# Optimization experiments

Hardware: AMD Instinct MI355X
Metric: run time of the kernel (lower is better)

The kernel has to match this reference:

```python
import jax, jax.numpy as jnp
import numpy as np

NUM_SLICES = 16
FEAT = 512  # last-dim size of input


def setup_inputs() -> dict:
    key = jax.random.key(0)
    k1, k2 = jax.random.split(key)
    input_tensor = jax.random.normal(k1, (2048, 64, FEAT), dtype=jnp.float32)
    # 16 slice start offsets, each slice of length 64 stays within FEAT
    slices_index = jnp.sort(jax.random.randint(k2, (NUM_SLICES,), 0, 448)).astype(jnp.int32)
    return {"input_tensor": input_tensor, "slices_index": slices_index, "slice_len": 64}


def reference(input_tensor, slices_index, slice_len):
    # Flatten all leading dims into rows, mirroring input_tensor.view(-1, sn)
    pre_dim = input_tensor.shape[:-1]
    n = input_tensor.shape[-1]
    x2 = input_tensor.reshape(-1, n)  # [R, N]
    # Gather indices for every (slice, position) pair: [K, L]
    idx = slices_index[:, None].astype(jnp.int32) + jnp.arange(slice_len, dtype=jnp.int32)[None, :]
    out = x2[:, idx]                      # [R, K, L]
    out = jnp.transpose(out, (1, 0, 2))   # [K, R, L] (slice-major, as fused_slice_low)
    return out.reshape((slices_index.shape[0],) + pre_dim + (slice_len,))
```

## Files before the change

### kernel.cpp

```cpp
#include <hip/hip_runtime.h>
#include <hip/hip_bf16.h>


#define ROWS   131072
#define FEATN  512
#define NSLICE 16
#define SLEN   64

typedef float vfloat4 __attribute__((ext_vector_type(4)));

__global__ __launch_bounds__(256) void fuse_slice_kernel(
    const float* __restrict__ in,
    const int*   __restrict__ sidx,
    float*       __restrict__ out)
{
    __shared__ float row[FEATN];
    __shared__ int   starts[NSLICE];

    const int r   = blockIdx.x;
    const int tid = threadIdx.x;

    const float2* in2 = reinterpret_cast<const float2*>(in + (size_t)r * FEATN);
    reinterpret_cast<float2*>(row)[tid] = in2[tid];
    if (tid < NSLICE) starts[tid] = sidx[tid];
    __syncthreads();

    const int s    = tid >> 4;
    const int c4   = (tid & 15) << 2;
    const int base = starts[s] + c4;

    vfloat4 v;
    v.x = row[base + 0];
    v.y = row[base + 1];
    v.z = row[base + 2];
    v.w = row[base + 3];

    vfloat4* outp = reinterpret_cast<vfloat4*>(
        out + ((size_t)s * ROWS + (size_t)r) * SLEN + c4);
    __builtin_nontemporal_store(v, outp);
}

extern "C" void kernel_launch(void* const* d_in, const int* in_sizes, int n_in,
                              void* d_out, int out_size, void* d_ws, size_t ws_size,
                              hipStream_t stream)
{
    const float* in   = reinterpret_cast<const float*>(d_in[0]);
    const int*   sidx = reinterpret_cast<const int*>(d_in[1]);
    float* out = reinterpret_cast<float*>(d_out);

    fuse_slice_kernel<<<ROWS, 256, 0, stream>>>(in, sidx, out);
}
```

Baseline: 681.4 us.

## Use persistent grid with direct global gathers instead of LDS row staging

Replaces one-block-per-row LDS staging with a grid-stride persistent kernel where each wave handles four slices and each 16-lane group one row, loading slice elements directly from global memory. This removes the shared-memory round trip, the barrier, the per-block launch overhead and reads of row columns outside any slice. It trades these for more unaligned scalar global loads that rely on cache for overlapping slices.

New measurement: 694.7 us. Within noise of the previous version (+2.0%).

```diff
diff --git a/kernel.cpp b/kernel.cpp
--- a/kernel.cpp
+++ b/kernel.cpp
@@ -1,11 +1,13 @@
 #include <hip/hip_runtime.h>
-#include <hip/hip_bf16.h>
 
 
 #define ROWS   131072
 #define FEATN  512
 #define NSLICE 16
 #define SLEN   64
+#define RPQ    4
+#define NQUAD  (ROWS / RPQ)
+#define GRID   2048
 
 typedef float vfloat4 __attribute__((ext_vector_type(4)));
 
@@ -14,30 +16,40 @@
     const int*   __restrict__ sidx,
     float*       __restrict__ out)
 {
-    __shared__ float row[FEATN];
-    __shared__ int   starts[NSLICE];
+    const int tid  = threadIdx.x;
+    const int wave = tid >> 6;
+    const int lane = tid & 63;
+    const int j    = lane >> 4;
+    const int l4   = (lane & 15) << 2;
 
-    const int r   = blockIdx.x;
-    const int tid = threadIdx.x;
+    int start[4];
+#pragma unroll
+    for (int k = 0; k < 4; ++k) start[k] = sidx[wave * 4 + k] + l4;
 
-    const float2* in2 = reinterpret_cast<const float2*>(in + (size_t)r * FEATN);
-    reinterpret_cast<float2*>(row)[tid] = in2[tid];
-    if (tid < NSLICE) starts[tid] = sidx[tid];
-    __syncthreads();
+    float* outb[4];
+#pragma unroll
+    for (int k = 0; k < 4; ++k)
+        outb[k] = out + ((size_t)(wave * 4 + k) * ROWS) * SLEN + l4;
 
-    const int s    = tid >> 4;
-    const int c4   = (tid & 15) << 2;
-    const int base = starts[s] + c4;
+    for (int q = blockIdx.x; q < NQUAD; q += GRID) {
+        const int r = q * RPQ + j;
+        const float* inr = in + (size_t)r * FEATN;
 
-    vfloat4 v;
-    v.x = row[base + 0];
-    v.y = row[base + 1];
-    v.z = row[base + 2];
-    v.w = row[base + 3];
+        vfloat4 v[4];
+#pragma unroll
+        for (int k = 0; k < 4; ++k) {
+            v[k].x = inr[start[k] + 0];
+            v[k].y = inr[start[k] + 1];
+            v[k].z = inr[start[k] + 2];
+            v[k].w = inr[start[k] + 3];
+        }
 
-    vfloat4* outp = reinterpret_cast<vfloat4*>(
-        out + ((size_t)s * ROWS + (size_t)r) * SLEN + c4);
-    __builtin_nontemporal_store(v, outp);
+#pragma unroll
+        for (int k = 0; k < 4; ++k) {
+            vfloat4* outp = reinterpret_cast<vfloat4*>(outb[k] + (size_t)r * SLEN);
+            __builtin_nontemporal_store(v[k], outp);
+        }
+    }
 }
 
 extern "C" void kernel_launch(void* const* d_in, const int* in_sizes, int n_in,
@@ -48,5 +60,5 @@
     const int*   sidx = reinterpret_cast<const int*>(d_in[1]);
     float* out = reinterpret_cast<float*>(d_out);
 
-    fuse_slice_kernel<<<ROWS, 256, 0, stream>>>(in, sidx, out);
+    fuse_slice_kernel<<<GRID, 256, 0, stream>>>(in, sidx, out);
 }
```
